# Kernel optimization log

Measured on AMD Instinct MI355X. Metric: run time of the kernel, lower is better.

The kernel has to match this reference:

```python
import jax, jax.numpy as jnp
from jax import lax
import numpy as np
import math

B, L, UNITS, DM, P = 2048, 2, 16, 512, 16
CH = UNITS // P            # 1  (attention 'head' dim c)
D = DM // P                # 32
C_ATT = CH * D             # 32 channels in patch space
C_FFN = 4 * C_ATT          # 128
HALF = P // 2              # 8 (post-stride-2 patch size)
EPS = 1e-5


def _to_patches(x):
    # 'b (c p1) (d p2) -> b (c d) p1 p2'
    b = x.shape[0]
    x = x.reshape(b, CH, P, D, P).transpose(0, 1, 3, 2, 4)
    return x.reshape(b, CH * D, P, P)


def _from_patches(x):
    # 'b (c d) p1 p2 -> b (c p1) (d p2)'
    b = x.shape[0]
    x = x.reshape(b, CH, D, P, P).transpose(0, 1, 3, 2, 4)
    return x.reshape(b, CH * P, D * P)


def _layernorm(x, g, b):
    m = jnp.mean(x, -1, keepdims=True)
    v = jnp.mean((x - m) ** 2, -1, keepdims=True)
    return (x - m) * lax.rsqrt(v + EPS) * g + b


def _dw_block(x, dw_w, dw_b, bn_g, bn_b, bn_m, bn_v, pw_w, pw_b, stride):
    # depthwise 3x3 conv -> BatchNorm (eval) -> 1x1 pointwise conv
    C = x.shape[1]
    y = lax.conv_general_dilated(
        x, dw_w[:, None], (stride, stride), [(1, 1), (1, 1)],
        dimension_numbers=('NCHW', 'OIHW', 'NCHW'), feature_group_count=C)
    if dw_b is not None:
        y = y + dw_b[None, :, None, None]
    scale = (bn_g * lax.rsqrt(bn_v + EPS))[None, :, None, None]
    y = (y - bn_m[None, :, None, None]) * scale + bn_b[None, :, None, None]
    y = jnp.einsum('bchw,oc->bohw', y, pw_w)
    if pw_b is not None:
        y = y + pw_b[None, :, None, None]
    return y


def _encoder(x, ln1_g, ln1_b, ln2_g, ln2_b, qkv_dw, qkv_bng, qkv_bnb, qkv_bnm,
             qkv_bnv, qkv_pw, position, c1d_w, c1d_b, lin_w, lin_b,
             f1_w, f1_b, fdw_w, fdw_b, f_bng, f_bnb, f_bnm, f_bnv,
             fpw_w, fpw_b, f2_w, f2_b):
    b = x.shape[0]
    for l in range(L):
        # ---- attention sublayer (pre-norm) ----
        x1 = _layernorm(x, ln1_g[l], ln1_b[l])
        xp = _to_patches(x1)                              # (B, 32, 16, 16)
        qkv = [_dw_block(xp, qkv_dw[l, i], None,
                         qkv_bng[l, i], qkv_bnb[l, i], qkv_bnm[l, i], qkv_bnv[l, i],
                         qkv_pw[l, i], None, 2)           # (B, 32, 8, 8)
               .reshape(b, CH, D, HALF * HALF)            # 'b (c d) p1 p2 -> b c d (p1 p2)'
               for i in range(3)]
        q, k, v = qkv
        scores = jnp.einsum('bcde,bcfe->bcdf', q, k) / math.sqrt(HALF * HALF)
        scores = scores + position[l][None]               # (B, 1, 32, 32)
        p_attn = jax.nn.softmax(scores, axis=-1)
        o = jnp.einsum('bcdf,bcfe->bcde', p_attn, v)      # (B, 1, 32, 64)
        # 'b c d (p1 p2) -> b (c p1) (d p2)' with p1 = P//2
        o = o.reshape(b, CH, D, HALF, HALF).transpose(0, 1, 3, 2, 4)
        o = o.reshape(b, CH * HALF, D * HALF)             # (B, 8, 256)
        o = jnp.einsum('bcd,oc->bod', o, c1d_w[l]) + c1d_b[l][None, :, None]
        o = jnp.einsum('bcd,od->bco', o, lin_w[l]) + lin_b[l]  # (B, 16, 512)
        x = x + o
        # ---- conv-FFN sublayer ----
        x2 = _layernorm(x, ln2_g[l], ln2_b[l])
        y = _to_patches(x2)                               # (B, 32, 16, 16)
        y = jnp.einsum('bchw,oc->bohw', y, f1_w[l]) + f1_b[l][None, :, None, None]
        y = jax.nn.relu(y)                                # (B, 128, 16, 16)
        y = _dw_block(y, fdw_w[l], fdw_b[l], f_bng[l], f_bnb[l], f_bnm[l],
                      f_bnv[l], fpw_w[l], fpw_b[l], 1)
        y = jax.nn.relu(y)
        y = jnp.einsum('bchw,oc->bohw', y, f2_w[l]) + f2_b[l][None, :, None, None]
        x = x + _from_patches(y)
    return x


def setup_inputs():
    key = jax.random.key(0)
    ks = iter(jax.random.split(key, 16))
    nrm = lambda shape, s=0.05: jax.random.normal(next(ks), shape, jnp.float32) * s
    return dict(
        x=jax.random.normal(next(ks), (B, UNITS, DM), jnp.float32),
        ln1_g=jnp.ones((L, DM)), ln1_b=jnp.zeros((L, DM)),
        ln2_g=jnp.ones((L, DM)), ln2_b=jnp.zeros((L, DM)),
        qkv_dw=nrm((L, 3, C_ATT, 3, 3)),
        qkv_bng=jnp.ones((L, 3, C_ATT)), qkv_bnb=jnp.zeros((L, 3, C_ATT)),
        qkv_bnm=jnp.zeros((L, 3, C_ATT)), qkv_bnv=jnp.ones((L, 3, C_ATT)),
        qkv_pw=nrm((L, 3, C_ATT, C_ATT)),
        position=nrm((L, CH, D, D), 1.0),
        c1d_w=nrm((L, UNITS, UNITS // 2)), c1d_b=jnp.zeros((L, UNITS)),
        lin_w=nrm((L, DM, DM // 2)), lin_b=jnp.zeros((L, DM)),
        f1_w=nrm((L, C_FFN, C_ATT)), f1_b=jnp.zeros((L, C_FFN)),
        fdw_w=nrm((L, C_FFN, 3, 3)), fdw_b=jnp.zeros((L, C_FFN)),
        f_bng=jnp.ones((L, C_FFN)), f_bnb=jnp.zeros((L, C_FFN)),
        f_bnm=jnp.zeros((L, C_FFN)), f_bnv=jnp.ones((L, C_FFN)),
        fpw_w=nrm((L, C_FFN, C_FFN)), fpw_b=jnp.zeros((L, C_FFN)),
        f2_w=nrm((L, C_ATT, C_FFN)), f2_b=jnp.zeros((L, C_ATT)),
    )


def reference(x, ln1_g, ln1_b, ln2_g, ln2_b, qkv_dw, qkv_bng, qkv_bnb, qkv_bnm,
              qkv_bnv, qkv_pw, position, c1d_w, c1d_b, lin_w, lin_b,
              f1_w, f1_b, fdw_w, fdw_b, f_bng, f_bnb, f_bnm, f_bnv,
              fpw_w, fpw_b, f2_w, f2_b):
    return _encoder(x, ln1_g, ln1_b, ln2_g, ln2_b, qkv_dw, qkv_bng, qkv_bnb,
                    qkv_bnm, qkv_bnv, qkv_pw, position, c1d_w, c1d_b, lin_w,
                    lin_b, f1_w, f1_b, fdw_w, fdw_b, f_bng, f_bnb, f_bnm,
                    f_bnv, fpw_w, fpw_b, f2_w, f2_b)
```

## Files before the change

### kernel.cpp

```cpp
#include <hip/hip_runtime.h>
#include <hip/hip_bf16.h>

#define B_ 2048
#define EPSF 1e-5f

typedef __attribute__((ext_vector_type(8))) short short8v;
typedef __attribute__((ext_vector_type(4))) short short4v;
typedef __attribute__((ext_vector_type(4))) float f32x4;

__device__ __forceinline__ short f2bf_s(float f) {
  union { float f; unsigned u; } v; v.f = f;
  unsigned r = v.u + 0x7fffu + ((v.u >> 16) & 1u);
  return (short)(r >> 16);
}
__device__ __forceinline__ float bf2f(short s) {
  return __uint_as_float(((unsigned)(unsigned short)s) << 16);
}

__global__ __launch_bounds__(256) void k_prep(
    const float* __restrict__ f1_w, const float* __restrict__ fpw_w,
    const float* __restrict__ f2_w, const float* __restrict__ qkv_pw,
    const float* __restrict__ lin_w, short* __restrict__ f1wb,
    short* __restrict__ img, short* __restrict__ qkvA,
    short* __restrict__ linb) {
  int i = blockIdx.x * 256 + threadIdx.x;
  if (i < 10240) {
    int l = i / 5120, r = i % 5120, o = r / 40, kk = r % 40;
    f1wb[i] = (kk < 32) ? f2bf_s(f1_w[l * 4096 + o * 32 + kk]) : (short)0;
  }
  if (i < 43520) {
    int l = i / 21760, r = i % 21760;
    short val;
    if (r < 17408) {
      int o = r / 136, kk = r % 136;
      val = (kk < 128) ? f2bf_s(fpw_w[l * 16384 + o * 128 + kk]) : (short)0;
    } else {
      int r2 = r - 17408;
      int d = r2 / 136, kk = r2 % 136;
      val = (kk < 128) ? f2bf_s(f2_w[l * 4096 + d * 128 + kk]) : (short)0;
    }
    img[l * 21760 + r] = val;
  }
  if (i < 7680) {
    int l = i / 3840, r = i % 3840;
    int io = r / 40, c = r % 40;
    qkvA[i] = (c < 32) ? f2bf_s(qkv_pw[l * 3072 + io * 32 + c]) : (short)0;
  }
  if (i < 262144) linb[i] = f2bf_s(lin_w[i]);
}

__device__ __forceinline__ void ln_to_patches(const float* __restrict__ xb,
                                              const float* __restrict__ g,
                                              const float* __restrict__ beta,
                                              float (*p)[257], int tid) {
  int lane = tid & 63, wave = tid >> 6;
  for (int r = wave; r < 16; r += 4) {
    float vals[8];
    float s = 0.f, ss = 0.f;
#pragma unroll
    for (int j = 0; j < 8; j++) {
      float t = xb[r * 512 + lane + j * 64];
      vals[j] = t; s += t; ss += t * t;
    }
#pragma unroll
    for (int o = 32; o; o >>= 1) { s += __shfl_xor(s, o); ss += __shfl_xor(ss, o); }
    float m = s * (1.f / 512.f);
    float inv = rsqrtf(ss * (1.f / 512.f) - m * m + EPSF);
#pragma unroll
    for (int j = 0; j < 8; j++) {
      int col = lane + j * 64;
      p[col >> 4][r * 16 + (col & 15)] = (vals[j] - m) * inv * g[col] + beta[col];
    }
  }
}

__global__ __launch_bounds__(256) void k_att(
    const float* __restrict__ x, const float* __restrict__ g,
    const float* __restrict__ beta, const float* __restrict__ dw,
    const float* __restrict__ bng, const float* __restrict__ bnb,
    const float* __restrict__ bnm, const float* __restrict__ bnv,
    const short* __restrict__ qkvA, const float* __restrict__ posn,
    const float* __restrict__ c1w, const float* __restrict__ c1b,
    const short* __restrict__ linb, const float* __restrict__ lin_b,
    float* __restrict__ xg) {
  __shared__ __align__(16) char smem[62592];
  float (*p)[257] = (float(*)[257])smem;
  float* sc  = (float*)(smem + 0);
  short* pa  = (short*)(smem + 4224);
  short* ore = (short*)(smem + 6784);
  short* xc1 = (short*)(smem + 11008);
  short* t3s = (short*)(smem + 32896);
  short* qe  = (short*)(smem + 48256);
  short* ke  = (short*)(smem + 52864);
  short* vt  = (short*)(smem + 57472);

  int b = blockIdx.x, tid = threadIdx.x;
  int lane = tid & 63, wid = tid >> 6;
  int row = lane & 15, kg = lane >> 4;
  const float* xb = x + (size_t)b * 8192;

  ln_to_patches(xb, g, beta, p, tid);
  __syncthreads();

  {
    int c = tid & 31, oy = tid >> 5;
    float r0[16], r1[16], r2[16];
    int iy0 = 2 * oy - 1;
#pragma unroll
    for (int i = 0; i < 16; i++) {
      r0[i] = (iy0 >= 0) ? p[c][iy0 * 16 + i] : 0.f;
      r1[i] = p[c][(2 * oy) * 16 + i];
      r2[i] = p[c][(2 * oy + 1) * 16 + i];
    }
    for (int iw = 0; iw < 3; iw++) {
      const float* w9 = dw + iw * 288 + c * 9;
      float w00 = w9[0], w01 = w9[1], w02 = w9[2];
      float w10 = w9[3], w11 = w9[4], w12 = w9[5];
      float w20 = w9[6], w21 = w9[7], w22 = w9[8];
      float scale = bng[iw * 32 + c] * rsqrtf(bnv[iw * 32 + c] + EPSF);
      float shift = bnb[iw * 32 + c] - bnm[iw * 32 + c] * scale;
#pragma unroll
      for (int ox = 0; ox < 8; ox++) {
        int ix = 2 * ox;
        float acc = w01 * r0[ix] + w11 * r1[ix] + w21 * r2[ix]
                  + w02 * r0[ix + 1] + w12 * r1[ix + 1] + w22 * r2[ix + 1];
        if (ix > 0) acc += w00 * r0[ix - 1] + w10 * r1[ix - 1] + w20 * r2[ix - 1];
        t3s[(iw * 64 + oy * 8 + ox) * 40 + c] = f2bf_s(acc * scale + shift);
      }
    }
  }
  __syncthreads();

  {
    int mi = wid & 1, nbase = (wid >> 1) * 2;
    for (int iw = 0; iw < 3; iw++) {
      short8v a = *(const short8v*)&qkvA[(iw * 32 + mi * 16 + row) * 40 + kg * 8];
      short8v b0 = *(const short8v*)&t3s[(iw * 64 + (nbase + 0) * 16 + row) * 40 + kg * 8];
      short8v b1 = *(const short8v*)&t3s[(iw * 64 + (nbase + 1) * 16 + row) * 40 + kg * 8];
      f32x4 z = {};
      f32x4 acc0 = __builtin_amdgcn_mfma_f32_16x16x32_bf16(a, b0, z, 0, 0, 0);
      f32x4 acc1 = __builtin_amdgcn_mfma_f32_16x16x32_bf16(a, b1, z, 0, 0, 0);
      if (iw < 2) {
        short* tgt = (iw == 0) ? qe : ke;
#pragma unroll
        for (int r = 0; r < 4; r++) {
          int d = mi * 16 + kg * 4 + r;
          tgt[d * 72 + (nbase + 0) * 16 + row] = f2bf_s(acc0[r]);
          tgt[d * 72 + (nbase + 1) * 16 + row] = f2bf_s(acc1[r]);
        }
      } else {
        int e0 = (nbase + 0) * 16 + row, e1 = (nbase + 1) * 16 + row;
        int fb = mi * 16 + kg * 4;
        short4v v0, v1;
        v0.x = f2bf_s(acc0[0]); v0.y = f2bf_s(acc0[1]);
        v0.z = f2bf_s(acc0[2]); v0.w = f2bf_s(acc0[3]);
        v1.x = f2bf_s(acc1[0]); v1.y = f2bf_s(acc1[1]);
        v1.z = f2bf_s(acc1[2]); v1.w = f2bf_s(acc1[3]);
        *(short4v*)&vt[e0 * 40 + fb] = v0;
        *(short4v*)&vt[e1 * 40 + fb] = v1;
      }
    }
  }
  __syncthreads();

  {
    int mi = wid & 1, ni = wid >> 1;
    f32x4 acc = {};
#pragma unroll
    for (int kk = 0; kk < 2; kk++) {
      short8v a = *(const short8v*)&qe[(mi * 16 + row) * 72 + kk * 32 + kg * 8];
      short8v bb = *(const short8v*)&ke[(ni * 16 + row) * 72 + kk * 32 + kg * 8];
      acc = __builtin_amdgcn_mfma_f32_16x16x32_bf16(a, bb, acc, 0, 0, 0);
    }
#pragma unroll
    for (int r = 0; r < 4; r++) {
      int d = mi * 16 + kg * 4 + r, f = ni * 16 + row;
      sc[d * 33 + f] = acc[r] * 0.125f + posn[d * 32 + f];
    }
  }
  __syncthreads();

  {
    int srow = tid >> 3, sg = tid & 7;
    float v0 = sc[srow * 33 + sg * 4 + 0];
    float v1 = sc[srow * 33 + sg * 4 + 1];
    float v2 = sc[srow * 33 + sg * 4 + 2];
    float v3 = sc[srow * 33 + sg * 4 + 3];
    float mx = fmaxf(fmaxf(v0, v1), fmaxf(v2, v3));
    mx = fmaxf(mx, __shfl_xor(mx, 1));
    mx = fmaxf(mx, __shfl_xor(mx, 2));
    mx = fmaxf(mx, __shfl_xor(mx, 4));
    float e0 = __expf(v0 - mx), e1 = __expf(v1 - mx);
    float e2 = __expf(v2 - mx), e3 = __expf(v3 - mx);
    float s = e0 + e1 + e2 + e3;
    s += __shfl_xor(s, 1); s += __shfl_xor(s, 2); s += __shfl_xor(s, 4);
    float inv = 1.f / s;
    short4v pk;
    pk.x = f2bf_s(e0 * inv); pk.y = f2bf_s(e1 * inv);
    pk.z = f2bf_s(e2 * inv); pk.w = f2bf_s(e3 * inv);
    *(short4v*)&pa[srow * 40 + sg * 4] = pk;
  }
  __syncthreads();

  {
    int mi = wid & 1, nbase = (wid >> 1) * 2;
    short8v a = *(const short8v*)&pa[(mi * 16 + row) * 40 + kg * 8];
#pragma unroll
    for (int t = 0; t < 2; t++) {
      int e = (nbase + t) * 16 + row;
      short8v bb = *(const short8v*)&vt[e * 40 + kg * 8];
      f32x4 z = {};
      f32x4 acc = __builtin_amdgcn_mfma_f32_16x16x32_bf16(a, bb, z, 0, 0, 0);
#pragma unroll
      for (int r = 0; r < 4; r++) {
        int d = mi * 16 + kg * 4 + r;
        ore[(e >> 3) * 264 + d * 8 + (e & 7)] = f2bf_s(acc[r]);
      }
    }
  }
  __syncthreads();

  {
    int n = tid;
#pragma unroll
    for (int u = 0; u < 16; u++) {
      float acc = c1b[u];
#pragma unroll
      for (int c = 0; c < 8; c++)
        acc += c1w[u * 8 + c] * bf2f(ore[c * 264 + n]);
      xc1[u * 264 + n] = f2bf_s(acc);
    }
  }
  __syncthreads();

  {
    short8v a8[8];
#pragma unroll
    for (int kk = 0; kk < 8; kk++)
      a8[kk] = *(const short8v*)&xc1[row * 264 + kk * 32 + kg * 8];
    float* xo = xg + (size_t)b * 8192;
    for (int t = 0; t < 8; t++) {
      int nt = wid * 8 + t;
      const short* bb_base = linb + (nt * 16 + row) * 256 + kg * 8;
      f32x4 acc = {};
#pragma unroll
      for (int kk = 0; kk < 8; kk++) {
        short8v bb = *(const short8v*)(bb_base + kk * 32);
        acc = __builtin_amdgcn_mfma_f32_16x16x32_bf16(a8[kk], bb, acc, 0, 0, 0);
      }
      int m = nt * 16 + row;
      float lb = lin_b[m];
#pragma unroll
      for (int r = 0; r < 4; r++) {
        int u = kg * 4 + r;
        xo[u * 512 + m] += acc[r] + lb;
      }
    }
  }
}

#define OFF_P   0
#define OFF_F1W 20480
#define OFF_T   0
#define OFF_Y   69632
__global__ __launch_bounds__(512) void k_ffn2(
    const float* __restrict__ x, const float* __restrict__ g,
    const float* __restrict__ beta, const short* __restrict__ f1wb,
    const float* __restrict__ f1b, const float* __restrict__ dww,
    const float* __restrict__ dwb, const float* __restrict__ bng,
    const float* __restrict__ bnb, const float* __restrict__ bnm,
    const float* __restrict__ bnv, const short* __restrict__ img,
    const float* __restrict__ pwb, const float* __restrict__ f2b,
    float* __restrict__ xg) {
  __shared__ __align__(16) char smem[137216];
  short* p_lds = (short*)(smem + OFF_P);
  short* f1w_lds = (short*)(smem + OFF_F1W);
  short* sT = (short*)(smem + OFF_T);
  short* sY = (short*)(smem + OFF_Y);
  short* pw_lds = (short*)(smem + OFF_Y);
  short* f2w_lds = (short*)(smem + OFF_Y + 34816);
  float* f2out = (float*)(smem + OFF_Y);

  int b = blockIdx.x, tid = threadIdx.x;
  int lane = tid & 63, wid = tid >> 6;
  int row = lane & 15, kg = lane >> 4;
  const float* xb = x + (size_t)b * 8192;

  const uint4* imgu = (const uint4*)img;
  uint4 pf0 = imgu[tid], pf1 = imgu[tid + 512], pf2 = imgu[tid + 1024];
  uint4 pf3 = imgu[tid + 1536], pf4 = imgu[tid + 2048];
  uint4 pf5 = {};
  if (tid < 160) pf5 = imgu[tid + 2560];

  {
    const uint4* src = (const uint4*)f1wb;
    uint4* dst = (uint4*)f1w_lds;
    dst[tid >= 512 ? 0 : tid] = src[tid >= 512 ? 0 : tid];
    if (tid < 128) dst[tid + 512] = src[tid + 512];
  }

  for (int r = wid; r < 16; r += 8) {
    float vals[8];
    float s = 0.f, ss = 0.f;
#pragma unroll
    for (int j = 0; j < 8; j++) {
      float t = xb[r * 512 + lane + j * 64];
      vals[j] = t; s += t; ss += t * t;
    }
#pragma unroll
    for (int o = 32; o; o >>= 1) { s += __shfl_xor(s, o); ss += __shfl_xor(ss, o); }
    float m = s * (1.f / 512.f);
    float inv = rsqrtf(ss * (1.f / 512.f) - m * m + EPSF);
#pragma unroll
    for (int j = 0; j < 8; j++) {
      int col = lane + j * 64;
      float nv = (vals[j] - m) * inv * g[col] + beta[col];
      p_lds[(r * 16 + (col & 15)) * 40 + (col >> 4)] = f2bf_s(nv);
    }
  }
  __syncthreads();

  {
    int o0 = (wid & 1) * 64, pos0 = (wid >> 1) * 64;
    f32x4 acc[4][4] = {};
    short8v a[4], bb[4];
#pragma unroll
    for (int mi = 0; mi < 4; mi++)
      a[mi] = *(const short8v*)&f1w_lds[(o0 + mi * 16 + row) * 40 + kg * 8];
#pragma unroll
    for (int ni = 0; ni < 4; ni++)
      bb[ni] = *(const short8v*)&p_lds[(pos0 + ni * 16 + row) * 40 + kg * 8];
#pragma unroll
    for (int mi = 0; mi < 4; mi++)
#pragma unroll
      for (int ni = 0; ni < 4; ni++)
        acc[mi][ni] = __builtin_amdgcn_mfma_f32_16x16x32_bf16(a[mi], bb[ni], acc[mi][ni], 0, 0, 0);
#pragma unroll
    for (int mi = 0; mi < 4; mi++) {
      int obase = o0 + mi * 16 + kg * 4;
      float b0 = f1b[obase], b1 = f1b[obase + 1], b2 = f1b[obase + 2], b3 = f1b[obase + 3];
#pragma unroll
      for (int ni = 0; ni < 4; ni++) {
        int pos = pos0 + ni * 16 + row;
        sY[(obase + 0) * 264 + pos] = f2bf_s(fmaxf(acc[mi][ni][0] + b0, 0.f));
        sY[(obase + 1) * 264 + pos] = f2bf_s(fmaxf(acc[mi][ni][1] + b1, 0.f));
        sY[(obase + 2) * 264 + pos] = f2bf_s(fmaxf(acc[mi][ni][2] + b2, 0.f));
        sY[(obase + 3) * 264 + pos] = f2bf_s(fmaxf(acc[mi][ni][3] + b3, 0.f));
      }
    }
  }
  __syncthreads();

  {
    int c = tid & 127, hb = tid >> 7;
    float wgt[3][3];
#pragma unroll
    for (int rr = 0; rr < 3; rr++)
#pragma unroll
      for (int kx = 0; kx < 3; kx++) wgt[rr][kx] = dww[c * 9 + rr * 3 + kx];
    float bias = dwb[c];
    float scale = bng[c] * rsqrtf(bnv[c] + EPSF);
    float shift = bnb[c] - bnm[c] * scale;
#pragma unroll
    for (int j = 0; j < 4; j++) {
      int h = hb * 4 + j;
      float fr0[18], fr1[18], fr2[18];
#pragma unroll
      for (int i = 0; i < 18; i++) { fr0[i] = 0.f; fr1[i] = 0.f; fr2[i] = 0.f; }
      if (h > 0) {
        short8v s0 = *(const short8v*)&sY[c * 264 + (h - 1) * 16];
        short8v s1 = *(const short8v*)&sY[c * 264 + (h - 1) * 16 + 8];
#pragma unroll
        for (int i = 0; i < 8; i++) { fr0[1 + i] = bf2f(s0[i]); fr0[9 + i] = bf2f(s1[i]); }
      }
      {
        short8v s0 = *(const short8v*)&sY[c * 264 + h * 16];
        short8v s1 = *(const short8v*)&sY[c * 264 + h * 16 + 8];
#pragma unroll
        for (int i = 0; i < 8; i++) { fr1[1 + i] = bf2f(s0[i]); fr1[9 + i] = bf2f(s1[i]); }
      }
      if (h < 15) {
        short8v s0 = *(const short8v*)&sY[c * 264 + (h + 1) * 16];
        short8v s1 = *(const short8v*)&sY[c * 264 + (h + 1) * 16 + 8];
#pragma unroll
        for (int i = 0; i < 8; i++) { fr2[1 + i] = bf2f(s0[i]); fr2[9 + i] = bf2f(s1[i]); }
      }
#pragma unroll
      for (int w = 0; w < 16; w++) {
        float acc = bias;
#pragma unroll
        for (int kx = 0; kx < 3; kx++) {
          acc += wgt[0][kx] * fr0[w + kx];
          acc += wgt[1][kx] * fr1[w + kx];
          acc += wgt[2][kx] * fr2[w + kx];
        }
        sT[(h * 16 + w) * 136 + c] = f2bf_s(acc * scale + shift);
      }
    }
  }
  __syncthreads();

  {
    uint4* wdst = (uint4*)pw_lds;
    wdst[tid] = pf0; wdst[tid + 512] = pf1; wdst[tid + 1024] = pf2;
    wdst[tid + 1536] = pf3; wdst[tid + 2048] = pf4;
    if (tid < 160) wdst[tid + 2560] = pf5;
  }
  __syncthreads();

  int o0 = (wid & 1) * 64, pos0 = (wid >> 1) * 64;
  f32x4 acc[4][4] = {};
#pragma unroll
  for (int kk = 0; kk < 4; kk++) {
    int k0 = kk * 32 + kg * 8;
    short8v a[4], bb[4];
#pragma unroll
    for (int mi = 0; mi < 4; mi++)
      a[mi] = *(const short8v*)&pw_lds[(o0 + mi * 16 + row) * 136 + k0];
#pragma unroll
    for (int ni = 0; ni < 4; ni++)
      bb[ni] = *(const short8v*)&sT[(pos0 + ni * 16 + row) * 136 + k0];
#pragma unroll
    for (int mi = 0; mi < 4; mi++)
#pragma unroll
      for (int ni = 0; ni < 4; ni++)
        acc[mi][ni] = __builtin_amdgcn_mfma_f32_16x16x32_bf16(a[mi], bb[ni], acc[mi][ni], 0, 0, 0);
  }
  __syncthreads();

#pragma unroll
  for (int mi = 0; mi < 4; mi++) {
    int obase = o0 + mi * 16 + kg * 4;
    float pb0 = pwb[obase], pb1 = pwb[obase + 1], pb2 = pwb[obase + 2], pb3 = pwb[obase + 3];
#pragma unroll
    for (int ni = 0; ni < 4; ni++) {
      int pos = pos0 + ni * 16 + row;
      short4v pk;
      pk.x = f2bf_s(fmaxf(acc[mi][ni][0] + pb0, 0.f));
      pk.y = f2bf_s(fmaxf(acc[mi][ni][1] + pb1, 0.f));
      pk.z = f2bf_s(fmaxf(acc[mi][ni][2] + pb2, 0.f));
      pk.w = f2bf_s(fmaxf(acc[mi][ni][3] + pb3, 0.f));
      *(short4v*)&sT[pos * 136 + obase] = pk;
    }
  }
  __syncthreads();

  {
    f32x4 acc2[2][2] = {};
    int nbase = wid * 2;
#pragma unroll
    for (int kk = 0; kk < 4; kk++) {
      int k0 = kk * 32 + kg * 8;
      short8v a2[2], b2[2];
#pragma unroll
      for (int mi = 0; mi < 2; mi++)
        a2[mi] = *(const short8v*)&f2w_lds[(mi * 16 + row) * 136 + k0];
#pragma unroll
      for (int ni = 0; ni < 2; ni++)
        b2[ni] = *(const short8v*)&sT[((nbase + ni) * 16 + row) * 136 + k0];
#pragma unroll
      for (int mi = 0; mi < 2; mi++)
#pragma unroll
        for (int ni = 0; ni < 2; ni++)
          acc2[mi][ni] = __builtin_amdgcn_mfma_f32_16x16x32_bf16(a2[mi], b2[ni], acc2[mi][ni], 0, 0, 0);
    }
#pragma unroll
    for (int mi = 0; mi < 2; mi++)
#pragma unroll
      for (int ni = 0; ni < 2; ni++) {
        int pos = (nbase + ni) * 16 + row;
        int dbase = mi * 16 + kg * 4;
        f2out[(dbase + 0) * 257 + pos] = acc2[mi][ni][0];
        f2out[(dbase + 1) * 257 + pos] = acc2[mi][ni][1];
        f2out[(dbase + 2) * 257 + pos] = acc2[mi][ni][2];
        f2out[(dbase + 3) * 257 + pos] = acc2[mi][ni][3];
      }
  }
  __syncthreads();

  float* xo = xg + (size_t)b * 8192;
#pragma unroll
  for (int j = 0; j < 16; j++) {
    int idx = tid + j * 512;
    int dm = idx & 511;
    int d = dm >> 4, p2 = dm & 15;
    int p1 = idx >> 9;
    xo[idx] += f2out[d * 257 + p1 * 16 + p2] + f2b[d];
  }
}

extern "C" void kernel_launch(void* const* d_in, const int* in_sizes, int n_in,
                              void* d_out, int out_size, void* d_ws, size_t ws_size,
                              hipStream_t stream) {
  const float* x_in   = (const float*)d_in[0];
  const float* ln1_g  = (const float*)d_in[1];
  const float* ln1_b  = (const float*)d_in[2];
  const float* ln2_g  = (const float*)d_in[3];
  const float* ln2_b  = (const float*)d_in[4];
  const float* qkv_dw = (const float*)d_in[5];
  const float* qkv_bng = (const float*)d_in[6];
  const float* qkv_bnb = (const float*)d_in[7];
  const float* qkv_bnm = (const float*)d_in[8];
  const float* qkv_bnv = (const float*)d_in[9];
  const float* qkv_pw = (const float*)d_in[10];
  const float* position = (const float*)d_in[11];
  const float* c1d_w  = (const float*)d_in[12];
  const float* c1d_b  = (const float*)d_in[13];
  const float* lin_w  = (const float*)d_in[14];
  const float* lin_b  = (const float*)d_in[15];
  const float* f1_w   = (const float*)d_in[16];
  const float* f1_b   = (const float*)d_in[17];
  const float* fdw_w  = (const float*)d_in[18];
  const float* fdw_b  = (const float*)d_in[19];
  const float* f_bng  = (const float*)d_in[20];
  const float* f_bnb  = (const float*)d_in[21];
  const float* f_bnm  = (const float*)d_in[22];
  const float* f_bnv  = (const float*)d_in[23];
  const float* fpw_w  = (const float*)d_in[24];
  const float* fpw_b  = (const float*)d_in[25];
  const float* f2_w   = (const float*)d_in[26];
  const float* f2_b   = (const float*)d_in[27];

  float* xbuf = (float*)d_out;
  short* f1wb = (short*)d_ws;
  short* img  = f1wb + 10240;
  short* qkvA = img + 43520;
  short* linb = qkvA + 7680;

  hipMemcpyAsync(xbuf, x_in, (size_t)B_ * 8192 * sizeof(float),
                 hipMemcpyDeviceToDevice, stream);
  k_prep<<<1024, 256, 0, stream>>>(f1_w, fpw_w, f2_w, qkv_pw, lin_w,
                                   f1wb, img, qkvA, linb);
  for (int l = 0; l < 2; l++) {
    k_att<<<B_, 256, 0, stream>>>(xbuf, ln1_g + l * 512, ln1_b + l * 512,
        qkv_dw + l * 864, qkv_bng + l * 96, qkv_bnb + l * 96,
        qkv_bnm + l * 96, qkv_bnv + l * 96, qkvA + l * 3840,
        position + l * 1024, c1d_w + l * 128, c1d_b + l * 16,
        linb + l * 131072, lin_b + l * 512, xbuf);
    k_ffn2<<<B_, 512, 0, stream>>>(xbuf, ln2_g + l * 512, ln2_b + l * 512,
        f1wb + l * 5120, f1_b + l * 128, fdw_w + l * 1152, fdw_b + l * 128,
        f_bng + l * 128, f_bnb + l * 128, f_bnm + l * 128, f_bnv + l * 128,
        img + l * 21760, fpw_b + l * 128, f2_b + l * 32, xbuf);
  }
}
```

Baseline: 427.1 us.

## Split FFN kernel into two row-halves to cut shared memory and raise occupancy

The FFN kernel is rewritten to process the 16x16 patch grid in two halves, each with a one-row halo. This shrinks shared memory from about 134KB to 70KB so several blocks can share a CU (launch bounds now request 4). Weights are read directly from global/L1 instead of being staged in LDS. Depthwise conv weights are pre-fused with BatchNorm in the prep kernel, and the pointwise buffers use an XOR-swizzled layout. The cost is recomputing f1 for the halo rows, extra barriers, and scattered uncoalesced global read-modify-writes to the output.

Result: slower. 779.1 us (+82.4%).

```diff
diff --git a/kernel.cpp b/kernel.cpp
--- a/kernel.cpp
+++ b/kernel.cpp
@@ -20,33 +20,32 @@
 __global__ __launch_bounds__(256) void k_prep(
     const float* __restrict__ f1_w, const float* __restrict__ fpw_w,
     const float* __restrict__ f2_w, const float* __restrict__ qkv_pw,
-    const float* __restrict__ lin_w, short* __restrict__ f1wb,
-    short* __restrict__ img, short* __restrict__ qkvA,
-    short* __restrict__ linb) {
+    const float* __restrict__ lin_w, const float* __restrict__ fdw_w,
+    const float* __restrict__ fdw_b, const float* __restrict__ f_bng,
+    const float* __restrict__ f_bnb, const float* __restrict__ f_bnm,
+    const float* __restrict__ f_bnv, short* __restrict__ qkvA,
+    short* __restrict__ linb, short* __restrict__ f1wb,
+    short* __restrict__ pwb, short* __restrict__ f2wb,
+    float* __restrict__ convW, float* __restrict__ convB) {
   int i = blockIdx.x * 256 + threadIdx.x;
-  if (i < 10240) {
-    int l = i / 5120, r = i % 5120, o = r / 40, kk = r % 40;
-    f1wb[i] = (kk < 32) ? f2bf_s(f1_w[l * 4096 + o * 32 + kk]) : (short)0;
-  }
-  if (i < 43520) {
-    int l = i / 21760, r = i % 21760;
-    short val;
-    if (r < 17408) {
-      int o = r / 136, kk = r % 136;
-      val = (kk < 128) ? f2bf_s(fpw_w[l * 16384 + o * 128 + kk]) : (short)0;
-    } else {
-      int r2 = r - 17408;
-      int d = r2 / 136, kk = r2 % 136;
-      val = (kk < 128) ? f2bf_s(f2_w[l * 4096 + d * 128 + kk]) : (short)0;
-    }
-    img[l * 21760 + r] = val;
-  }
   if (i < 7680) {
     int l = i / 3840, r = i % 3840;
     int io = r / 40, c = r % 40;
     qkvA[i] = (c < 32) ? f2bf_s(qkv_pw[l * 3072 + io * 32 + c]) : (short)0;
   }
   if (i < 262144) linb[i] = f2bf_s(lin_w[i]);
+  if (i < 8192) f1wb[i] = f2bf_s(f1_w[i]);
+  if (i < 32768) pwb[i] = f2bf_s(fpw_w[i]);
+  if (i < 8192) f2wb[i] = f2bf_s(f2_w[i]);
+  if (i < 256) {
+    int l = i >> 7, c = i & 127;
+    float scale = f_bng[l * 128 + c] * rsqrtf(f_bnv[l * 128 + c] + EPSF);
+#pragma unroll
+    for (int k = 0; k < 9; k++)
+      convW[l * 1152 + k * 128 + c] = fdw_w[(l * 128 + c) * 9 + k] * scale;
+    convB[l * 128 + c] =
+        (fdw_b[l * 128 + c] - f_bnm[l * 128 + c]) * scale + f_bnb[l * 128 + c];
+  }
 }
 
 __device__ __forceinline__ void ln_to_patches(const float* __restrict__ xb,
@@ -259,52 +258,30 @@
   }
 }
 
-#define OFF_P   0
-#define OFF_F1W 20480
-#define OFF_T   0
-#define OFF_Y   69632
-__global__ __launch_bounds__(512) void k_ffn2(
+__global__ __launch_bounds__(512, 4) void k_ffn3(
     const float* __restrict__ x, const float* __restrict__ g,
-    const float* __restrict__ beta, const short* __restrict__ f1wb,
-    const float* __restrict__ f1b, const float* __restrict__ dww,
-    const float* __restrict__ dwb, const float* __restrict__ bng,
-    const float* __restrict__ bnb, const float* __restrict__ bnm,
-    const float* __restrict__ bnv, const short* __restrict__ img,
-    const float* __restrict__ pwb, const float* __restrict__ f2b,
-    float* __restrict__ xg) {
-  __shared__ __align__(16) char smem[137216];
-  short* p_lds = (short*)(smem + OFF_P);
-  short* f1w_lds = (short*)(smem + OFF_F1W);
-  short* sT = (short*)(smem + OFF_T);
-  short* sY = (short*)(smem + OFF_Y);
-  short* pw_lds = (short*)(smem + OFF_Y);
-  short* f2w_lds = (short*)(smem + OFF_Y + 34816);
-  float* f2out = (float*)(smem + OFF_Y);
+    const float* __restrict__ beta, const short* __restrict__ f1wg,
+    const float* __restrict__ f1b, const float* __restrict__ convW,
+    const float* __restrict__ convB, const short* __restrict__ pwg,
+    const float* __restrict__ pwbias, const short* __restrict__ f2wg,
+    const float* __restrict__ f2b, float* __restrict__ xg) {
+  __shared__ __align__(16) char smem[71680];
+  short* sY = (short*)smem;
+  char* sTB = smem + 38912;
+  short* pP = (short*)(smem + 38912);
 
   int b = blockIdx.x, tid = threadIdx.x;
   int lane = tid & 63, wid = tid >> 6;
   int row = lane & 15, kg = lane >> 4;
   const float* xb = x + (size_t)b * 8192;
-
-  const uint4* imgu = (const uint4*)img;
-  uint4 pf0 = imgu[tid], pf1 = imgu[tid + 512], pf2 = imgu[tid + 1024];
-  uint4 pf3 = imgu[tid + 1536], pf4 = imgu[tid + 2048];
-  uint4 pf5 = {};
-  if (tid < 160) pf5 = imgu[tid + 2560];
-
-  {
-    const uint4* src = (const uint4*)f1wb;
-    uint4* dst = (uint4*)f1w_lds;
-    dst[tid >= 512 ? 0 : tid] = src[tid >= 512 ? 0 : tid];
-    if (tid < 128) dst[tid + 512] = src[tid + 512];
-  }
-
-  for (int r = wid; r < 16; r += 8) {
+  float* xo = xg + (size_t)b * 8192;
+
+  for (int rr = wid; rr < 16; rr += 8) {
     float vals[8];
     float s = 0.f, ss = 0.f;
 #pragma unroll
     for (int j = 0; j < 8; j++) {
-      float t = xb[r * 512 + lane + j * 64];
+      float t = xb[rr * 512 + lane + j * 64];
       vals[j] = t; s += t; ss += t * t;
     }
 #pragma unroll
@@ -315,177 +292,152 @@
     for (int j = 0; j < 8; j++) {
       int col = lane + j * 64;
       float nv = (vals[j] - m) * inv * g[col] + beta[col];
-      p_lds[(r * 16 + (col & 15)) * 40 + (col >> 4)] = f2bf_s(nv);
-    }
-  }
-  __syncthreads();
-
-  {
-    int o0 = (wid & 1) * 64, pos0 = (wid >> 1) * 64;
-    f32x4 acc[4][4] = {};
-    short8v a[4], bb[4];
-#pragma unroll
-    for (int mi = 0; mi < 4; mi++)
-      a[mi] = *(const short8v*)&f1w_lds[(o0 + mi * 16 + row) * 40 + kg * 8];
-#pragma unroll
-    for (int ni = 0; ni < 4; ni++)
-      bb[ni] = *(const short8v*)&p_lds[(pos0 + ni * 16 + row) * 40 + kg * 8];
-#pragma unroll
-    for (int mi = 0; mi < 4; mi++)
-#pragma unroll
-      for (int ni = 0; ni < 4; ni++)
-        acc[mi][ni] = __builtin_amdgcn_mfma_f32_16x16x32_bf16(a[mi], bb[ni], acc[mi][ni], 0, 0, 0);
-#pragma unroll
-    for (int mi = 0; mi < 4; mi++) {
-      int obase = o0 + mi * 16 + kg * 4;
-      float b0 = f1b[obase], b1 = f1b[obase + 1], b2 = f1b[obase + 2], b3 = f1b[obase + 3];
+      pP[(rr * 16 + (col & 15)) * 32 + (col >> 4)] = f2bf_s(nv);
+    }
+  }
+  __syncthreads();
+  uint4 st0 = ((const uint4*)pP)[2 * tid];
+  uint4 st1 = ((const uint4*)pP)[2 * tid + 1];
+
+  for (int ph = 0; ph < 2; ++ph) {
+    if (ph) {
+      __syncthreads();
+      ((uint4*)pP)[2 * tid] = st0;
+      ((uint4*)pP)[2 * tid + 1] = st1;
+    }
+    __syncthreads();
+
+    {
+      int o0 = (wid & 1) * 64;
+      for (int tt = (wid >> 1); tt < 9; tt += 4) {
+        int rg = (ph ? 7 : 0) + tt;
+        short8v bb = *(const short8v*)&pP[(rg * 16 + row) * 32 + kg * 8];
+        short8v a0 = *(const short8v*)&f1wg[(o0 + 0 * 16 + row) * 32 + kg * 8];
+        short8v a1 = *(const short8v*)&f1wg[(o0 + 1 * 16 + row) * 32 + kg * 8];
+        short8v a2 = *(const short8v*)&f1wg[(o0 + 2 * 16 + row) * 32 + kg * 8];
+        short8v a3 = *(const short8v*)&f1wg[(o0 + 3 * 16 + row) * 32 + kg * 8];
+        f32x4 z = {};
+        f32x4 c0 = __builtin_amdgcn_mfma_f32_16x16x32_bf16(a0, bb, z, 0, 0, 0);
+        f32x4 c1 = __builtin_amdgcn_mfma_f32_16x16x32_bf16(a1, bb, z, 0, 0, 0);
+        f32x4 c2 = __builtin_amdgcn_mfma_f32_16x16x32_bf16(a2, bb, z, 0, 0, 0);
+        f32x4 c3 = __builtin_amdgcn_mfma_f32_16x16x32_bf16(a3, bb, z, 0, 0, 0);
+#pragma unroll
+        for (int mi = 0; mi < 4; mi++) {
+          f32x4 cc = (mi == 0) ? c0 : (mi == 1) ? c1 : (mi == 2) ? c2 : c3;
+          int ob = o0 + mi * 16 + kg * 4;
+#pragma unroll
+          for (int r2 = 0; r2 < 4; r2++) {
+            int c = ob + r2;
+            sY[c * 152 + tt * 16 + row] = f2bf_s(fmaxf(cc[r2] + f1b[c], 0.f));
+          }
+        }
+      }
+    }
+    __syncthreads();
+
+    {
+      int c = tid & 127, hb = tid >> 7;
+      float w_[9];
+#pragma unroll
+      for (int k = 0; k < 9; k++) w_[k] = convW[k * 128 + c];
+      float cb = convB[c];
+      int rlo = ph ? 7 : 0;
+#pragma unroll
+      for (int j = 0; j < 2; j++) {
+        int hl = hb * 2 + j;
+        int h = ph * 8 + hl;
+        float acc[16];
+#pragma unroll
+        for (int w = 0; w < 16; w++) acc[w] = cb;
+#pragma unroll
+        for (int rr = 0; rr < 3; rr++) {
+          int rg = h - 1 + rr;
+          if (rg < 0 || rg > 15) continue;
+          int rl = rg - rlo;
+          short8v s0 = *(const short8v*)&sY[c * 152 + rl * 16];
+          short8v s1 = *(const short8v*)&sY[c * 152 + rl * 16 + 8];
+          float f[18];
+          f[0] = 0.f; f[17] = 0.f;
+#pragma unroll
+          for (int i = 0; i < 8; i++) { f[1 + i] = bf2f(s0[i]); f[9 + i] = bf2f(s1[i]); }
+          float w0 = w_[rr * 3], w1 = w_[rr * 3 + 1], w2 = w_[rr * 3 + 2];
+#pragma unroll
+          for (int w = 0; w < 16; w++)
+            acc[w] += w0 * f[w] + w1 * f[w + 1] + w2 * f[w + 2];
+        }
+#pragma unroll
+        for (int w = 0; w < 16; w++) {
+          int pos = hl * 16 + w;
+          int byte = ((pos * 128 + c) * 2) ^ ((pos & 7) << 4);
+          *(short*)(sTB + byte) = f2bf_s(acc[w]);
+        }
+      }
+    }
+    __syncthreads();
+
+    int o0 = (wid & 3) * 32, pos0 = (wid >> 2) * 64;
+    f32x4 facc[2][4] = {};
+#pragma unroll
+    for (int kk = 0; kk < 4; kk++) {
+      short8v a0 = *(const short8v*)&pwg[(o0 + row) * 128 + kk * 32 + kg * 8];
+      short8v a1 = *(const short8v*)&pwg[(o0 + 16 + row) * 128 + kk * 32 + kg * 8];
+      short8v bb[4];
 #pragma unroll
       for (int ni = 0; ni < 4; ni++) {
         int pos = pos0 + ni * 16 + row;
-        sY[(obase + 0) * 264 + pos] = f2bf_s(fmaxf(acc[mi][ni][0] + b0, 0.f));
-        sY[(obase + 1) * 264 + pos] = f2bf_s(fmaxf(acc[mi][ni][1] + b1, 0.f));
-        sY[(obase + 2) * 264 + pos] = f2bf_s(fmaxf(acc[mi][ni][2] + b2, 0.f));
-        sY[(obase + 3) * 264 + pos] = f2bf_s(fmaxf(acc[mi][ni][3] + b3, 0.f));
-      }
-    }
-  }
-  __syncthreads();
-
-  {
-    int c = tid & 127, hb = tid >> 7;
-    float wgt[3][3];
-#pragma unroll
-    for (int rr = 0; rr < 3; rr++)
-#pragma unroll
-      for (int kx = 0; kx < 3; kx++) wgt[rr][kx] = dww[c * 9 + rr * 3 + kx];
-    float bias = dwb[c];
-    float scale = bng[c] * rsqrtf(bnv[c] + EPSF);
-    float shift = bnb[c] - bnm[c] * scale;
-#pragma unroll
-    for (int j = 0; j < 4; j++) {
-      int h = hb * 4 + j;
-      float fr0[18], fr1[18], fr2[18];
-#pragma unroll
-      for (int i = 0; i < 18; i++) { fr0[i] = 0.f; fr1[i] = 0.f; fr2[i] = 0.f; }
-      if (h > 0) {
-        short8v s0 = *(const short8v*)&sY[c * 264 + (h - 1) * 16];
-        short8v s1 = *(const short8v*)&sY[c * 264 + (h - 1) * 16 + 8];
-#pragma unroll
-        for (int i = 0; i < 8; i++) { fr0[1 + i] = bf2f(s0[i]); fr0[9 + i] = bf2f(s1[i]); }
-      }
-      {
-        short8v s0 = *(const short8v*)&sY[c * 264 + h * 16];
-        short8v s1 = *(const short8v*)&sY[c * 264 + h * 16 + 8];
-#pragma unroll
-        for (int i = 0; i < 8; i++) { fr1[1 + i] = bf2f(s0[i]); fr1[9 + i] = bf2f(s1[i]); }
-      }
-      if (h < 15) {
-        short8v s0 = *(const short8v*)&sY[c * 264 + (h + 1) * 16];
-        short8v s1 = *(const short8v*)&sY[c * 264 + (h + 1) * 16 + 8];
-#pragma unroll
-        for (int i = 0; i < 8; i++) { fr2[1 + i] = bf2f(s0[i]); fr2[9 + i] = bf2f(s1[i]); }
-      }
-#pragma unroll
-      for (int w = 0; w < 16; w++) {
-        float acc = bias;
-#pragma unroll
-        for (int kx = 0; kx < 3; kx++) {
-          acc += wgt[0][kx] * fr0[w + kx];
-          acc += wgt[1][kx] * fr1[w + kx];
-          acc += wgt[2][kx] * fr2[w + kx];
+        int byte = ((pos * 128 + kk * 32 + kg * 8) * 2) ^ ((pos & 7) << 4);
+        bb[ni] = *(const short8v*)(sTB + byte);
+      }
+#pragma unroll
+      for (int ni = 0; ni < 4; ni++) {
+        facc[0][ni] = __builtin_amdgcn_mfma_f32_16x16x32_bf16(a0, bb[ni], facc[0][ni], 0, 0, 0);
+        facc[1][ni] = __builtin_amdgcn_mfma_f32_16x16x32_bf16(a1, bb[ni], facc[1][ni], 0, 0, 0);
+      }
+    }
+    __syncthreads();
+
+#pragma unroll
+    for (int mi = 0; mi < 2; mi++) {
+      int ob = o0 + mi * 16 + kg * 4;
+      float pb0 = pwbias[ob], pb1 = pwbias[ob + 1];
+      float pb2 = pwbias[ob + 2], pb3 = pwbias[ob + 3];
+#pragma unroll
+      for (int ni = 0; ni < 4; ni++) {
+        int pos = pos0 + ni * 16 + row;
+        short4v pk;
+        pk.x = f2bf_s(fmaxf(facc[mi][ni][0] + pb0, 0.f));
+        pk.y = f2bf_s(fmaxf(facc[mi][ni][1] + pb1, 0.f));
+        pk.z = f2bf_s(fmaxf(facc[mi][ni][2] + pb2, 0.f));
+        pk.w = f2bf_s(fmaxf(facc[mi][ni][3] + pb3, 0.f));
+        int byte = ((pos * 128 + ob) * 2) ^ ((pos & 7) << 4);
+        *(short4v*)(sTB + byte) = pk;
+      }
+    }
+    __syncthreads();
+
+    {
+      f32x4 acc2[2] = {};
+      int pos0f = wid * 16;
+      int pos = pos0f + row;
+#pragma unroll
+      for (int kk = 0; kk < 4; kk++) {
+        short8v a0 = *(const short8v*)&f2wg[(row) * 128 + kk * 32 + kg * 8];
+        short8v a1 = *(const short8v*)&f2wg[(16 + row) * 128 + kk * 32 + kg * 8];
+        int byte = ((pos * 128 + kk * 32 + kg * 8) * 2) ^ ((pos & 7) << 4);
+        short8v bb = *(const short8v*)(sTB + byte);
+        acc2[0] = __builtin_amdgcn_mfma_f32_16x16x32_bf16(a0, bb, acc2[0], 0, 0, 0);
+        acc2[1] = __builtin_amdgcn_mfma_f32_16x16x32_bf16(a1, bb, acc2[1], 0, 0, 0);
+      }
+      int pos_g = ph * 128 + pos;
+      int p1 = pos_g >> 4, p2 = pos_g & 15;
+#pragma unroll
+      for (int mi = 0; mi < 2; mi++)
+#pragma unroll
+        for (int r2 = 0; r2 < 4; r2++) {
+          int d = mi * 16 + kg * 4 + r2;
+          xo[p1 * 512 + d * 16 + p2] += acc2[mi][r2] + f2b[d];
         }
-        sT[(h * 16 + w) * 136 + c] = f2bf_s(acc * scale + shift);
-      }
-    }
-  }
-  __syncthreads();
-
-  {
-    uint4* wdst = (uint4*)pw_lds;
-    wdst[tid] = pf0; wdst[tid + 512] = pf1; wdst[tid + 1024] = pf2;
-    wdst[tid + 1536] = pf3; wdst[tid + 2048] = pf4;
-    if (tid < 160) wdst[tid + 2560] = pf5;
-  }
-  __syncthreads();
-
-  int o0 = (wid & 1) * 64, pos0 = (wid >> 1) * 64;
-  f32x4 acc[4][4] = {};
-#pragma unroll
-  for (int kk = 0; kk < 4; kk++) {
-    int k0 = kk * 32 + kg * 8;
-    short8v a[4], bb[4];
-#pragma unroll
-    for (int mi = 0; mi < 4; mi++)
-      a[mi] = *(const short8v*)&pw_lds[(o0 + mi * 16 + row) * 136 + k0];
-#pragma unroll
-    for (int ni = 0; ni < 4; ni++)
-      bb[ni] = *(const short8v*)&sT[(pos0 + ni * 16 + row) * 136 + k0];
-#pragma unroll
-    for (int mi = 0; mi < 4; mi++)
-#pragma unroll
-      for (int ni = 0; ni < 4; ni++)
-        acc[mi][ni] = __builtin_amdgcn_mfma_f32_16x16x32_bf16(a[mi], bb[ni], acc[mi][ni], 0, 0, 0);
-  }
-  __syncthreads();
-
-#pragma unroll
-  for (int mi = 0; mi < 4; mi++) {
-    int obase = o0 + mi * 16 + kg * 4;
-    float pb0 = pwb[obase], pb1 = pwb[obase + 1], pb2 = pwb[obase + 2], pb3 = pwb[obase + 3];
-#pragma unroll
-    for (int ni = 0; ni < 4; ni++) {
-      int pos = pos0 + ni * 16 + row;
-      short4v pk;
-      pk.x = f2bf_s(fmaxf(acc[mi][ni][0] + pb0, 0.f));
-      pk.y = f2bf_s(fmaxf(acc[mi][ni][1] + pb1, 0.f));
-      pk.z = f2bf_s(fmaxf(acc[mi][ni][2] + pb2, 0.f));
-      pk.w = f2bf_s(fmaxf(acc[mi][ni][3] + pb3, 0.f));
-      *(short4v*)&sT[pos * 136 + obase] = pk;
-    }
-  }
-  __syncthreads();
-
-  {
-    f32x4 acc2[2][2] = {};
-    int nbase = wid * 2;
-#pragma unroll
-    for (int kk = 0; kk < 4; kk++) {
-      int k0 = kk * 32 + kg * 8;
-      short8v a2[2], b2[2];
-#pragma unroll
-      for (int mi = 0; mi < 2; mi++)
-        a2[mi] = *(const short8v*)&f2w_lds[(mi * 16 + row) * 136 + k0];
-#pragma unroll
-      for (int ni = 0; ni < 2; ni++)
-        b2[ni] = *(const short8v*)&sT[((nbase + ni) * 16 + row) * 136 + k0];
-#pragma unroll
-      for (int mi = 0; mi < 2; mi++)
-#pragma unroll
-        for (int ni = 0; ni < 2; ni++)
-          acc2[mi][ni] = __builtin_amdgcn_mfma_f32_16x16x32_bf16(a2[mi], b2[ni], acc2[mi][ni], 0, 0, 0);
-    }
-#pragma unroll
-    for (int mi = 0; mi < 2; mi++)
-#pragma unroll
-      for (int ni = 0; ni < 2; ni++) {
-        int pos = (nbase + ni) * 16 + row;
-        int dbase = mi * 16 + kg * 4;
-        f2out[(dbase + 0) * 257 + pos] = acc2[mi][ni][0];
-        f2out[(dbase + 1) * 257 + pos] = acc2[mi][ni][1];
-        f2out[(dbase + 2) * 257 + pos] = acc2[mi][ni][2];
-        f2out[(dbase + 3) * 257 + pos] = acc2[mi][ni][3];
-      }
-  }
-  __syncthreads();
-
-  float* xo = xg + (size_t)b * 8192;
-#pragma unroll
-  for (int j = 0; j < 16; j++) {
-    int idx = tid + j * 512;
-    int dm = idx & 511;
-    int d = dm >> 4, p2 = dm & 15;
-    int p1 = idx >> 9;
-    xo[idx] += f2out[d * 257 + p1 * 16 + p2] + f2b[d];
+    }
   }
 }
 
@@ -522,24 +474,27 @@
   const float* f2_b   = (const float*)d_in[27];
 
   float* xbuf = (float*)d_out;
-  short* f1wb = (short*)d_ws;
-  short* img  = f1wb + 10240;
-  short* qkvA = img + 43520;
+  short* qkvA = (short*)d_ws;
   short* linb = qkvA + 7680;
+  short* f1wb = linb + 262144;
+  short* pwb  = f1wb + 8192;
+  short* f2wb = pwb + 32768;
+  float* convW = (float*)(f2wb + 8192);
+  float* convB = convW + 2304;
 
   hipMemcpyAsync(xbuf, x_in, (size_t)B_ * 8192 * sizeof(float),
                  hipMemcpyDeviceToDevice, stream);
   k_prep<<<1024, 256, 0, stream>>>(f1_w, fpw_w, f2_w, qkv_pw, lin_w,
-                                   f1wb, img, qkvA, linb);
+      fdw_w, fdw_b, f_bng, f_bnb, f_bnm, f_bnv,
+      qkvA, linb, f1wb, pwb, f2wb, convW, convB);
   for (int l = 0; l < 2; l++) {
     k_att<<<B_, 256, 0, stream>>>(xbuf, ln1_g + l * 512, ln1_b + l * 512,
         qkv_dw + l * 864, qkv_bng + l * 96, qkv_bnb + l * 96,
         qkv_bnm + l * 96, qkv_bnv + l * 96, qkvA + l * 3840,
         position + l * 1024, c1d_w + l * 128, c1d_b + l * 16,
         linb + l * 131072, lin_b + l * 512, xbuf);
-    k_ffn2<<<B_, 512, 0, stream>>>(xbuf, ln2_g + l * 512, ln2_b + l * 512,
-        f1wb + l * 5120, f1_b + l * 128, fdw_w + l * 1152, fdw_b + l * 128,
-        f_bng + l * 128, f_bnb + l * 128, f_bnm + l * 128, f_bnv + l * 128,
-        img + l * 21760, fpw_b + l * 128, f2_b + l * 32, xbuf);
-  }
-}
+    k_ffn3<<<B_, 512, 0, stream>>>(xbuf, ln2_g + l * 512, ln2_b + l * 512,
+        f1wb + l * 4096, f1_b + l * 128, convW + l * 1152, convB + l * 128,
+        pwb + l * 16384, fpw_b + l * 128, f2wb + l * 4096, f2_b + l * 32, xbuf);
+  }
+}
```
